# Performance work log

Hardware: AMD Instinct MI355X
Metric: run time of the kernel (lower is better)

## Reference

```python
import jax, jax.numpy as jnp
import numpy as np
from jax import lax

B, C, H, W = 16, 256, 64, 64
K = 3  # kernel_size


def setup_inputs() -> dict:
    key = jax.random.key(0)
    k1, k2, k3, k4 = jax.random.split(key, 4)
    x = jax.random.normal(k1, (B, C, H, W), dtype=jnp.float32)
    # nn.Parameter init is ones; perturb so softmax is non-trivial
    dir_weight_h = jnp.ones((1, C, 1, 1), jnp.float32) + 0.1 * jax.random.normal(k2, (1, C, 1, 1), jnp.float32)
    dir_weight_w = jnp.ones((1, C, 1, 1), jnp.float32) + 0.1 * jax.random.normal(k3, (1, C, 1, 1), jnp.float32)
    gate_w = 0.1 * jax.random.normal(k4, (), jnp.float32)  # 1x1 conv on 1 channel = scalar
    gate_b = jnp.float32(-1.0)  # init.constant_(gate.bias, -1.0)
    return {"x": x, "dir_weight_h": dir_weight_h, "dir_weight_w": dir_weight_w,
            "gate_w": gate_w, "gate_b": gate_b}


def reference(x, dir_weight_h, dir_weight_w, gate_w, gate_b):
    b, c, h, w = x.shape
    # directional softmax-weighted global pooling
    ww = jax.nn.softmax(dir_weight_w, axis=1)            # (1,C,1,1)
    global_h = jnp.mean(x * ww, axis=3, keepdims=True)   # (B,C,H,1)
    wh = jax.nn.softmax(dir_weight_h, axis=1)
    global_w = jnp.mean(x * wh, axis=2, keepdims=True)   # (B,C,1,W)
    global_dir = global_h + global_w                     # broadcast -> (B,C,H,W)

    # local covariance: unfold(x1)*unfold(x2) mean over k*k taps
    # == KxK box-sum of (x1*x2) with zero padding, divided by k*k
    half = c // 2
    prod = x[:, :half] * x[:, half:]                     # (B,C/2,H,W)
    cov = lax.reduce_window(prod, 0.0, lax.add,
                            window_dimensions=(1, 1, K, K),
                            window_strides=(1, 1, 1, 1),
                            padding=[(0, 0), (0, 0), (K // 2, K // 2), (K // 2, K // 2)]) / (K * K)

    consistency = jnp.mean(jnp.abs(cov), axis=1, keepdims=True)  # (B,1,H,W)
    local_anomaly = 1.0 - jnp.clip(consistency, 0.0, 1.0)

    fusion = jnp.mean(global_dir, axis=1, keepdims=True) * local_anomaly  # (B,1,H,W)
    attention = jax.nn.sigmoid(gate_w * fusion + gate_b)  # 1x1 conv with scalar weight/bias
    return x * attention
```

## Files before the change

kernel.cpp:

```cpp
#include <hip/hip_runtime.h>
#include <math.h>

#define NB 16
#define NC 256
#define NH 64
#define NW 64
#define HALF 128
#define PLANE (NH*NW)

#define WS_ATT 0

#define SCR_CONS 0
#define SCR_GHP  524288
#define SCR_GWP  (524288 + 8192)

__device__ __forceinline__ float sum4(float4 v) { return (v.x+v.y)+(v.z+v.w); }

__global__ __launch_bounds__(256) void k_reduce(const float* __restrict__ x,
                                                const float* __restrict__ dwh,
                                                const float* __restrict__ dww,
                                                float* __restrict__ scr) {
    __shared__ float  ew[256], eh[256];
    __shared__ float  wsum[8];
    __shared__ float4 consacc[4][8][16];
    __shared__ float  ghacc[4][8];
    __shared__ float  gwacc[4][64];

    const int t    = threadIdx.x;
    const int v    = t >> 6;
    const int lane = t & 63;
    const int pl   = lane & 3;
    const int w4   = lane >> 2;

    const int blk = blockIdx.x;
    const int hg  = blk & 7;
    const int cg  = (blk >> 3) & 7;
    const int b   = blk >> 6;
    const int r0  = hg << 3;

    {
        const float vw = dww[t], vh = dwh[t];
        const float evw = expf(vw), evh = expf(vh);
        ew[t] = evw; eh[t] = evh;
        float sw = evw, sh = evh;
        #pragma unroll
        for (int m = 1; m < 64; m <<= 1) { sw += __shfl_xor(sw, m); sh += __shfl_xor(sh, m); }
        if (lane == 0) { wsum[v] = sw; wsum[4+v] = sh; }
    }
    __syncthreads();
    const float invSw = 1.f/((wsum[0]+wsum[1])+(wsum[2]+wsum[3]));
    const float invSh = 1.f/((wsum[4]+wsum[5])+(wsum[6]+wsum[7]));

    const int   c1  = cg*16 + v*4 + pl;
    const float ww1 = ew[c1]*invSw, ww2 = ew[c1+HALF]*invSw;
    const float wh1 = eh[c1]*invSh, wh2 = eh[c1+HALF]*invSh;

    const float* p1 = x + ((size_t)(b*NC + c1))*PLANE + w4*4;
    const float* p2 = p1 + (size_t)HALF*PLANE;

    float4 w0 = {0,0,0,0}, w1 = {0,0,0,0}, w2 = {0,0,0,0};
    float4 colacc = {0,0,0,0};

    #pragma unroll
    for (int j = 0; j < 10; ++j) {
        const int r = r0 - 1 + j;
        float4 p = {0.f,0.f,0.f,0.f};
        const bool live = (j == 0) ? (r >= 0) : ((j == 9) ? (r < 64) : true);
        if (live) {
            const float4 x1 = *reinterpret_cast<const float4*>(p1 + r*NW);
            const float4 x2 = *reinterpret_cast<const float4*>(p2 + r*NW);
            p.x = x1.x*x2.x; p.y = x1.y*x2.y; p.z = x1.z*x2.z; p.w = x1.w*x2.w;
            if (j >= 1 && j <= 8) {
                float g = ww1*sum4(x1) + ww2*sum4(x2);
                g += __shfl_xor(g,1);  g += __shfl_xor(g,2);  g += __shfl_xor(g,4);
                g += __shfl_xor(g,8);  g += __shfl_xor(g,16); g += __shfl_xor(g,32);
                if (lane == 0) ghacc[v][j-1] = g;
                colacc.x += wh1*x1.x + wh2*x2.x;
                colacc.y += wh1*x1.y + wh2*x2.y;
                colacc.z += wh1*x1.z + wh2*x2.z;
                colacc.w += wh1*x1.w + wh2*x2.w;
            }
        }
        w0 = w1; w1 = w2; w2 = p;
        if (j >= 2) {
            float4 vs;
            vs.x = w0.x+w1.x+w2.x; vs.y = w0.y+w1.y+w2.y;
            vs.z = w0.z+w1.z+w2.z; vs.w = w0.w+w1.w+w2.w;
            float L = __shfl_up(vs.w, 4);
            float R = __shfl_down(vs.x, 4);
            if (w4 == 0)  L = 0.f;
            if (w4 == 15) R = 0.f;
            float4 c;
            c.x = fabsf(L    + vs.x + vs.y);
            c.y = fabsf(vs.x + vs.y + vs.z);
            c.z = fabsf(vs.y + vs.z + vs.w);
            c.w = fabsf(vs.z + vs.w + R);
            c.x += __shfl_xor(c.x,1); c.x += __shfl_xor(c.x,2);
            c.y += __shfl_xor(c.y,1); c.y += __shfl_xor(c.y,2);
            c.z += __shfl_xor(c.z,1); c.z += __shfl_xor(c.z,2);
            c.w += __shfl_xor(c.w,1); c.w += __shfl_xor(c.w,2);
            if (pl == 0) consacc[v][j-2][w4] = c;
        }
    }

    colacc.x += __shfl_xor(colacc.x,1); colacc.x += __shfl_xor(colacc.x,2);
    colacc.y += __shfl_xor(colacc.y,1); colacc.y += __shfl_xor(colacc.y,2);
    colacc.z += __shfl_xor(colacc.z,1); colacc.z += __shfl_xor(colacc.z,2);
    colacc.w += __shfl_xor(colacc.w,1); colacc.w += __shfl_xor(colacc.w,2);
    if (pl == 0) {
        gwacc[v][w4*4+0] = colacc.x;
        gwacc[v][w4*4+1] = colacc.y;
        gwacc[v][w4*4+2] = colacc.z;
        gwacc[v][w4*4+3] = colacc.w;
    }
    __syncthreads();

    const float SC  = 1.0f/(9.0f*128.0f);
    const float GSC = 1.0f/16384.0f;
    if (t < 128) {
        const int row = t >> 4, q = t & 15;
        const float4 s0 = consacc[0][row][q], s1 = consacc[1][row][q];
        const float4 s2 = consacc[2][row][q], s3 = consacc[3][row][q];
        float4 s;
        s.x = ((s0.x+s1.x)+(s2.x+s3.x))*SC;
        s.y = ((s0.y+s1.y)+(s2.y+s3.y))*SC;
        s.z = ((s0.z+s1.z)+(s2.z+s3.z))*SC;
        s.w = ((s0.w+s1.w)+(s2.w+s3.w))*SC;
        reinterpret_cast<float4*>(scr)[(cg << 14) + (b << 10) + (r0 + row)*16 + q] = s;
    } else if (t < 136) {
        const int row = t - 128;
        const float g = (ghacc[0][row]+ghacc[1][row])+(ghacc[2][row]+ghacc[3][row]);
        scr[SCR_GHP + (b*NH + r0 + row)*8 + cg] = g * GSC;
    } else if (t < 200) {
        const int w = t - 136;
        const float s = (gwacc[0][w]+gwacc[1][w])+(gwacc[2][w]+gwacc[3][w]);
        scr[SCR_GWP + (size_t)(b*NW + w)*64 + cg*8 + hg] = s * GSC;
    }
}

__global__ __launch_bounds__(256) void k_att(float* __restrict__ ws,
                                             const float* __restrict__ scr,
                                             const float* __restrict__ pgw,
                                             const float* __restrict__ pgb) {
    __shared__ __align__(16) float sgw[64];
    __shared__ __align__(16) float sgh[4];
    const int t = threadIdx.x;
    const int s = blockIdx.x & 15;
    const int b = blockIdx.x >> 4;

    if (t < 64) {
        const float4* gp = reinterpret_cast<const float4*>(scr + SCR_GWP + (size_t)(b*NW + t)*64);
        float acc = 0.f;
        #pragma unroll
        for (int i = 0; i < 16; ++i) acc += sum4(gp[i]);
        sgw[t] = acc;
    } else if (t < 68) {
        const int r = s*4 + (t - 64);
        const float4* gp = reinterpret_cast<const float4*>(scr + SCR_GHP + (b*NH + r)*8);
        sgh[t-64] = sum4(gp[0]) + sum4(gp[1]);
    }
    __syncthreads();

    if (t < 64) {
        const int u = (b << 10) + (s << 6) + t;
        const float4* cp = reinterpret_cast<const float4*>(scr);
        float4 sm = {0.f,0.f,0.f,0.f};
        #pragma unroll
        for (int g = 0; g < 8; ++g) {
            const float4 vv = cp[(g << 14) + u];
            sm.x += vv.x; sm.y += vv.y; sm.z += vv.z; sm.w += vv.w;
        }
        const float ghv  = sgh[t >> 4];
        const float4 gwv = *reinterpret_cast<const float4*>(&sgw[(t & 15)*4]);
        const float gW = pgw[0], gB = pgb[0];

        float4 o;
        float z;
        z = gW*(ghv+gwv.x)*(1.f - fminf(fmaxf(sm.x,0.f),1.f)) + gB; o.x = 1.f/(1.f+expf(-z));
        z = gW*(ghv+gwv.y)*(1.f - fminf(fmaxf(sm.y,0.f),1.f)) + gB; o.y = 1.f/(1.f+expf(-z));
        z = gW*(ghv+gwv.z)*(1.f - fminf(fmaxf(sm.z,0.f),1.f)) + gB; o.z = 1.f/(1.f+expf(-z));
        z = gW*(ghv+gwv.w)*(1.f - fminf(fmaxf(sm.w,0.f),1.f)) + gB; o.w = 1.f/(1.f+expf(-z));
        reinterpret_cast<float4*>(ws + WS_ATT)[u] = o;
    }
}

__global__ __launch_bounds__(256) void k_apply(const float* __restrict__ x,
                                               const float* __restrict__ ws,
                                               float* __restrict__ out) {
    const float* att = ws + WS_ATT;
    const int total4 = NB*NC*NH*NW/4;
    const int stride = gridDim.x * blockDim.x;
    for (int i = blockIdx.x*blockDim.x + threadIdx.x; i < total4; i += stride) {
        const int w4 = i & 15;
        const int h  = (i >> 4) & 63;
        const int b  = i >> 18;
        const float4 xv = reinterpret_cast<const float4*>(x)[i];
        const float4 av = reinterpret_cast<const float4*>(att)[(b << 10) + (h << 4) + w4];
        float4 o;
        o.x = xv.x*av.x; o.y = xv.y*av.y; o.z = xv.z*av.z; o.w = xv.w*av.w;
        reinterpret_cast<float4*>(out)[i] = o;
    }
}

extern "C" void kernel_launch(void* const* d_in, const int* in_sizes, int n_in,
                              void* d_out, int out_size, void* d_ws, size_t ws_size,
                              hipStream_t stream) {
    const float* x   = (const float*)d_in[0];
    const float* dwh = (const float*)d_in[1];
    const float* dww = (const float*)d_in[2];
    const float* pgw = (const float*)d_in[3];
    const float* pgb = (const float*)d_in[4];
    float* out = (float*)d_out;
    float* ws  = (float*)d_ws;
    float* scr = out;

    k_reduce<<<NB*8*8, 256, 0, stream>>>(x, dwh, dww, scr);
    k_att<<<256, 256, 0, stream>>>(ws, scr, pgw, pgb);
    k_apply<<<2048, 256, 0, stream>>>(x, ws, out);
}
```

Measured before the change: 43.68 us.

## Split channel pairs across lanes and double reduce grid to 2048 blocks

Each lane now loads one channel instead of both halves of a pair. The partner channel's value is obtained through a lane shuffle, and the per-block channel group shrinks from 16 to 8 channels. The reduce grid doubles to 2048 blocks to raise parallelism and memory-level concurrency on the first pass. In exchange, the scratch partial buffers and the attention kernel's reductions double in size (16 consistency groups, 128 column partials), which adds extra scratch traffic and shuffles.

```diff
diff --git a/kernel.cpp b/kernel.cpp
--- a/kernel.cpp
+++ b/kernel.cpp
@@ -11,8 +11,8 @@
 #define WS_ATT 0
 
 #define SCR_CONS 0
-#define SCR_GHP  524288
-#define SCR_GWP  (524288 + 8192)
+#define SCR_GHP  1048576
+#define SCR_GWP  (1048576 + 16384)
 
 __device__ __forceinline__ float sum4(float4 v) { return (v.x+v.y)+(v.z+v.w); }
 
@@ -29,13 +29,13 @@
     const int t    = threadIdx.x;
     const int v    = t >> 6;
     const int lane = t & 63;
-    const int pl   = lane & 3;
+    const int ch   = lane & 3;
     const int w4   = lane >> 2;
 
     const int blk = blockIdx.x;
     const int hg  = blk & 7;
-    const int cg  = (blk >> 3) & 7;
-    const int b   = blk >> 6;
+    const int cg  = (blk >> 3) & 15;
+    const int b   = blk >> 7;
     const int r0  = hg << 3;
 
     {
@@ -51,12 +51,11 @@
     const float invSw = 1.f/((wsum[0]+wsum[1])+(wsum[2]+wsum[3]));
     const float invSh = 1.f/((wsum[4]+wsum[5])+(wsum[6]+wsum[7]));
 
-    const int   c1  = cg*16 + v*4 + pl;
-    const float ww1 = ew[c1]*invSw, ww2 = ew[c1+HALF]*invSw;
-    const float wh1 = eh[c1]*invSh, wh2 = eh[c1+HALF]*invSh;
-
-    const float* p1 = x + ((size_t)(b*NC + c1))*PLANE + w4*4;
-    const float* p2 = p1 + (size_t)HALF*PLANE;
+    const int   c  = cg*8 + v*2 + (ch >> 1) + (ch & 1)*HALF;
+    const float wwc = ew[c]*invSw;
+    const float whc = eh[c]*invSh;
+
+    const float* pc = x + ((size_t)(b*NC + c))*PLANE + w4*4;
 
     float4 w0 = {0,0,0,0}, w1 = {0,0,0,0}, w2 = {0,0,0,0};
     float4 colacc = {0,0,0,0};
@@ -67,18 +66,20 @@
         float4 p = {0.f,0.f,0.f,0.f};
         const bool live = (j == 0) ? (r >= 0) : ((j == 9) ? (r < 64) : true);
         if (live) {
-            const float4 x1 = *reinterpret_cast<const float4*>(p1 + r*NW);
-            const float4 x2 = *reinterpret_cast<const float4*>(p2 + r*NW);
-            p.x = x1.x*x2.x; p.y = x1.y*x2.y; p.z = x1.z*x2.z; p.w = x1.w*x2.w;
+            const float4 xv = *reinterpret_cast<const float4*>(pc + r*NW);
+            float4 xp;
+            xp.x = __shfl_xor(xv.x, 1); xp.y = __shfl_xor(xv.y, 1);
+            xp.z = __shfl_xor(xv.z, 1); xp.w = __shfl_xor(xv.w, 1);
+            p.x = xv.x*xp.x; p.y = xv.y*xp.y; p.z = xv.z*xp.z; p.w = xv.w*xp.w;
             if (j >= 1 && j <= 8) {
-                float g = ww1*sum4(x1) + ww2*sum4(x2);
+                float g = wwc * sum4(xv);
                 g += __shfl_xor(g,1);  g += __shfl_xor(g,2);  g += __shfl_xor(g,4);
                 g += __shfl_xor(g,8);  g += __shfl_xor(g,16); g += __shfl_xor(g,32);
                 if (lane == 0) ghacc[v][j-1] = g;
-                colacc.x += wh1*x1.x + wh2*x2.x;
-                colacc.y += wh1*x1.y + wh2*x2.y;
-                colacc.z += wh1*x1.z + wh2*x2.z;
-                colacc.w += wh1*x1.w + wh2*x2.w;
+                colacc.x += whc*xv.x;
+                colacc.y += whc*xv.y;
+                colacc.z += whc*xv.z;
+                colacc.w += whc*xv.w;
             }
         }
         w0 = w1; w1 = w2; w2 = p;
@@ -90,16 +91,16 @@
             float R = __shfl_down(vs.x, 4);
             if (w4 == 0)  L = 0.f;
             if (w4 == 15) R = 0.f;
-            float4 c;
-            c.x = fabsf(L    + vs.x + vs.y);
-            c.y = fabsf(vs.x + vs.y + vs.z);
-            c.z = fabsf(vs.y + vs.z + vs.w);
-            c.w = fabsf(vs.z + vs.w + R);
-            c.x += __shfl_xor(c.x,1); c.x += __shfl_xor(c.x,2);
-            c.y += __shfl_xor(c.y,1); c.y += __shfl_xor(c.y,2);
-            c.z += __shfl_xor(c.z,1); c.z += __shfl_xor(c.z,2);
-            c.w += __shfl_xor(c.w,1); c.w += __shfl_xor(c.w,2);
-            if (pl == 0) consacc[v][j-2][w4] = c;
+            float4 cc;
+            cc.x = fabsf(L    + vs.x + vs.y);
+            cc.y = fabsf(vs.x + vs.y + vs.z);
+            cc.z = fabsf(vs.y + vs.z + vs.w);
+            cc.w = fabsf(vs.z + vs.w + R);
+            cc.x += __shfl_xor(cc.x,2);
+            cc.y += __shfl_xor(cc.y,2);
+            cc.z += __shfl_xor(cc.z,2);
+            cc.w += __shfl_xor(cc.w,2);
+            if (ch == 0) consacc[v][j-2][w4] = cc;
         }
     }
 
@@ -107,7 +108,7 @@
     colacc.y += __shfl_xor(colacc.y,1); colacc.y += __shfl_xor(colacc.y,2);
     colacc.z += __shfl_xor(colacc.z,1); colacc.z += __shfl_xor(colacc.z,2);
     colacc.w += __shfl_xor(colacc.w,1); colacc.w += __shfl_xor(colacc.w,2);
-    if (pl == 0) {
+    if (ch == 0) {
         gwacc[v][w4*4+0] = colacc.x;
         gwacc[v][w4*4+1] = colacc.y;
         gwacc[v][w4*4+2] = colacc.z;
@@ -130,11 +131,11 @@
     } else if (t < 136) {
         const int row = t - 128;
         const float g = (ghacc[0][row]+ghacc[1][row])+(ghacc[2][row]+ghacc[3][row]);
-        scr[SCR_GHP + (b*NH + r0 + row)*8 + cg] = g * GSC;
+        scr[SCR_GHP + (b*NH + r0 + row)*16 + cg] = g * GSC;
     } else if (t < 200) {
         const int w = t - 136;
         const float s = (gwacc[0][w]+gwacc[1][w])+(gwacc[2][w]+gwacc[3][w]);
-        scr[SCR_GWP + (size_t)(b*NW + w)*64 + cg*8 + hg] = s * GSC;
+        scr[SCR_GWP + (size_t)(b*NW + w)*128 + cg*8 + hg] = s * GSC;
     }
 }
 
@@ -149,15 +150,15 @@
     const int b = blockIdx.x >> 4;
 
     if (t < 64) {
-        const float4* gp = reinterpret_cast<const float4*>(scr + SCR_GWP + (size_t)(b*NW + t)*64);
+        const float4* gp = reinterpret_cast<const float4*>(scr + SCR_GWP + (size_t)(b*NW + t)*128);
         float acc = 0.f;
         #pragma unroll
-        for (int i = 0; i < 16; ++i) acc += sum4(gp[i]);
+        for (int i = 0; i < 32; ++i) acc += sum4(gp[i]);
         sgw[t] = acc;
     } else if (t < 68) {
         const int r = s*4 + (t - 64);
-        const float4* gp = reinterpret_cast<const float4*>(scr + SCR_GHP + (b*NH + r)*8);
-        sgh[t-64] = sum4(gp[0]) + sum4(gp[1]);
+        const float4* gp = reinterpret_cast<const float4*>(scr + SCR_GHP + (b*NH + r)*16);
+        sgh[t-64] = (sum4(gp[0]) + sum4(gp[1])) + (sum4(gp[2]) + sum4(gp[3]));
     }
     __syncthreads();
 
@@ -166,7 +167,7 @@
         const float4* cp = reinterpret_cast<const float4*>(scr);
         float4 sm = {0.f,0.f,0.f,0.f};
         #pragma unroll
-        for (int g = 0; g < 8; ++g) {
+        for (int g = 0; g < 16; ++g) {
             const float4 vv = cp[(g << 14) + u];
             sm.x += vv.x; sm.y += vv.y; sm.z += vv.z; sm.w += vv.w;
         }
@@ -214,7 +215,7 @@
     float* ws  = (float*)d_ws;
     float* scr = out;
 
-    k_reduce<<<NB*8*8, 256, 0, stream>>>(x, dwh, dww, scr);
+    k_reduce<<<NB*16*8, 256, 0, stream>>>(x, dwh, dww, scr);
     k_att<<<256, 256, 0, stream>>>(ws, scr, pgw, pgb);
     k_apply<<<2048, 256, 0, stream>>>(x, ws, out);
 }
```

Result: slower. 51.47 us (+17.8%).

## Restructure reduce kernel to process whole channel-pair planes per block via LDS stencil

Applied to the files above, without the earlier changes.

The reduce kernel now has each block process four full 64x64 channel-pair planes instead of an 8-row strip of 16 pairs. The horizontal 3-tap sum is done with lane shuffles, and the vertical sum goes through an LDS buffer. This removes halo row reloads and the per-row cross-lane reductions. The cost is four times more partial-sum planes in scratch, which the attention kernel now reduces over 32 groups, plus two barriers per plane.

```diff
diff --git a/kernel.cpp b/kernel.cpp
--- a/kernel.cpp
+++ b/kernel.cpp
@@ -7,36 +7,48 @@
 #define NW 64
 #define HALF 128
 #define PLANE (NH*NW)
+#define NPG 32
 
 #define WS_ATT 0
 
 #define SCR_CONS 0
-#define SCR_GHP  524288
-#define SCR_GWP  (524288 + 8192)
+#define SCR_GHP  2097152
+#define SCR_GWP  (2097152 + 32768)
+
+#define HPAD 76
 
 __device__ __forceinline__ float sum4(float4 v) { return (v.x+v.y)+(v.z+v.w); }
+
+__device__ __forceinline__ float4 hsum4(float4 p, int fc) {
+    float pl = __shfl_up(p.w, 1);
+    float pr = __shfl_down(p.x, 1);
+    if (fc == 0)  pl = 0.f;
+    if (fc == 15) pr = 0.f;
+    float4 h;
+    h.x = pl  + p.x + p.y;
+    h.y = p.x + p.y + p.z;
+    h.z = p.y + p.z + p.w;
+    h.w = p.z + p.w + pr;
+    return h;
+}
 
 __global__ __launch_bounds__(256) void k_reduce(const float* __restrict__ x,
                                                 const float* __restrict__ dwh,
                                                 const float* __restrict__ dww,
                                                 float* __restrict__ scr) {
-    __shared__ float  ew[256], eh[256];
-    __shared__ float  wsum[8];
-    __shared__ float4 consacc[4][8][16];
-    __shared__ float  ghacc[4][8];
-    __shared__ float  gwacc[4][64];
-
-    const int t    = threadIdx.x;
-    const int v    = t >> 6;
-    const int lane = t & 63;
-    const int pl   = lane & 3;
-    const int w4   = lane >> 2;
+    __shared__ float ew[256], eh[256];
+    __shared__ float wsum[8];
+    __shared__ float hs[64*HPAD];
+
+    const int t   = threadIdx.x;
+    const int v   = t >> 6;
+    const int lane= t & 63;
+    const int g16 = t >> 4;
+    const int w4  = t & 15;
 
     const int blk = blockIdx.x;
-    const int hg  = blk & 7;
-    const int cg  = (blk >> 3) & 7;
-    const int b   = blk >> 6;
-    const int r0  = hg << 3;
+    const int pg  = blk & (NPG-1);
+    const int b   = blk >> 5;
 
     {
         const float vw = dww[t], vh = dwh[t];
@@ -51,90 +63,118 @@
     const float invSw = 1.f/((wsum[0]+wsum[1])+(wsum[2]+wsum[3]));
     const float invSh = 1.f/((wsum[4]+wsum[5])+(wsum[6]+wsum[7]));
 
-    const int   c1  = cg*16 + v*4 + pl;
-    const float ww1 = ew[c1]*invSw, ww2 = ew[c1+HALF]*invSw;
-    const float wh1 = eh[c1]*invSh, wh2 = eh[c1+HALF]*invSh;
-
-    const float* p1 = x + ((size_t)(b*NC + c1))*PLANE + w4*4;
-    const float* p2 = p1 + (size_t)HALF*PLANE;
-
-    float4 w0 = {0,0,0,0}, w1 = {0,0,0,0}, w2 = {0,0,0,0};
+    float4 c4a0 = {0,0,0,0}, c4a1 = {0,0,0,0}, c4a2 = {0,0,0,0}, c4a3 = {0,0,0,0};
+    float  gh0 = 0.f, gh1 = 0.f, gh2 = 0.f, gh3 = 0.f;
     float4 colacc = {0,0,0,0};
+    float4* hsf4 = reinterpret_cast<float4*>(hs);
 
     #pragma unroll
-    for (int j = 0; j < 10; ++j) {
-        const int r = r0 - 1 + j;
-        float4 p = {0.f,0.f,0.f,0.f};
-        const bool live = (j == 0) ? (r >= 0) : ((j == 9) ? (r < 64) : true);
-        if (live) {
-            const float4 x1 = *reinterpret_cast<const float4*>(p1 + r*NW);
-            const float4 x2 = *reinterpret_cast<const float4*>(p2 + r*NW);
-            p.x = x1.x*x2.x; p.y = x1.y*x2.y; p.z = x1.z*x2.z; p.w = x1.w*x2.w;
-            if (j >= 1 && j <= 8) {
-                float g = ww1*sum4(x1) + ww2*sum4(x2);
-                g += __shfl_xor(g,1);  g += __shfl_xor(g,2);  g += __shfl_xor(g,4);
-                g += __shfl_xor(g,8);  g += __shfl_xor(g,16); g += __shfl_xor(g,32);
-                if (lane == 0) ghacc[v][j-1] = g;
-                colacc.x += wh1*x1.x + wh2*x2.x;
-                colacc.y += wh1*x1.y + wh2*x2.y;
-                colacc.z += wh1*x1.z + wh2*x2.z;
-                colacc.w += wh1*x1.w + wh2*x2.w;
-            }
-        }
-        w0 = w1; w1 = w2; w2 = p;
-        if (j >= 2) {
-            float4 vs;
-            vs.x = w0.x+w1.x+w2.x; vs.y = w0.y+w1.y+w2.y;
-            vs.z = w0.z+w1.z+w2.z; vs.w = w0.w+w1.w+w2.w;
-            float L = __shfl_up(vs.w, 4);
-            float R = __shfl_down(vs.x, 4);
-            if (w4 == 0)  L = 0.f;
-            if (w4 == 15) R = 0.f;
-            float4 c;
-            c.x = fabsf(L    + vs.x + vs.y);
-            c.y = fabsf(vs.x + vs.y + vs.z);
-            c.z = fabsf(vs.y + vs.z + vs.w);
-            c.w = fabsf(vs.z + vs.w + R);
-            c.x += __shfl_xor(c.x,1); c.x += __shfl_xor(c.x,2);
-            c.y += __shfl_xor(c.y,1); c.y += __shfl_xor(c.y,2);
-            c.z += __shfl_xor(c.z,1); c.z += __shfl_xor(c.z,2);
-            c.w += __shfl_xor(c.w,1); c.w += __shfl_xor(c.w,2);
-            if (pl == 0) consacc[v][j-2][w4] = c;
-        }
-    }
-
-    colacc.x += __shfl_xor(colacc.x,1); colacc.x += __shfl_xor(colacc.x,2);
-    colacc.y += __shfl_xor(colacc.y,1); colacc.y += __shfl_xor(colacc.y,2);
-    colacc.z += __shfl_xor(colacc.z,1); colacc.z += __shfl_xor(colacc.z,2);
-    colacc.w += __shfl_xor(colacc.w,1); colacc.w += __shfl_xor(colacc.w,2);
-    if (pl == 0) {
-        gwacc[v][w4*4+0] = colacc.x;
-        gwacc[v][w4*4+1] = colacc.y;
-        gwacc[v][w4*4+2] = colacc.z;
-        gwacc[v][w4*4+3] = colacc.w;
-    }
-    __syncthreads();
+    for (int pp = 0; pp < 4; ++pp) {
+        const int c1 = pg*4 + pp;
+        const float ww1 = ew[c1]*invSw, ww2 = ew[c1+HALF]*invSw;
+        const float wh1 = eh[c1]*invSh, wh2 = eh[c1+HALF]*invSh;
+
+        const float4* q1 = reinterpret_cast<const float4*>(x + ((size_t)(b*NC + c1))*PLANE);
+        const float4* q2 = reinterpret_cast<const float4*>(x + ((size_t)(b*NC + c1 + HALF))*PLANE);
+
+        const float4 a0 = q1[t], a1 = q1[t+256], a2 = q1[t+512], a3 = q1[t+768];
+        const float4 b0 = q2[t], b1 = q2[t+256], b2 = q2[t+512], b3 = q2[t+768];
+
+        gh0 += ww1*sum4(a0) + ww2*sum4(b0);
+        gh1 += ww1*sum4(a1) + ww2*sum4(b1);
+        gh2 += ww1*sum4(a2) + ww2*sum4(b2);
+        gh3 += ww1*sum4(a3) + ww2*sum4(b3);
+        colacc.x += wh1*((a0.x+a1.x)+(a2.x+a3.x)) + wh2*((b0.x+b1.x)+(b2.x+b3.x));
+        colacc.y += wh1*((a0.y+a1.y)+(a2.y+a3.y)) + wh2*((b0.y+b1.y)+(b2.y+b3.y));
+        colacc.z += wh1*((a0.z+a1.z)+(a2.z+a3.z)) + wh2*((b0.z+b1.z)+(b2.z+b3.z));
+        colacc.w += wh1*((a0.w+a1.w)+(a2.w+a3.w)) + wh2*((b0.w+b1.w)+(b2.w+b3.w));
+
+        float4 p, h;
+        p.x=a0.x*b0.x; p.y=a0.y*b0.y; p.z=a0.z*b0.z; p.w=a0.w*b0.w;
+        h = hsum4(p, w4); hsf4[(g16 +  0)*19 + w4] = h;
+        p.x=a1.x*b1.x; p.y=a1.y*b1.y; p.z=a1.z*b1.z; p.w=a1.w*b1.w;
+        h = hsum4(p, w4); hsf4[(g16 + 16)*19 + w4] = h;
+        p.x=a2.x*b2.x; p.y=a2.y*b2.y; p.z=a2.z*b2.z; p.w=a2.w*b2.w;
+        h = hsum4(p, w4); hsf4[(g16 + 32)*19 + w4] = h;
+        p.x=a3.x*b3.x; p.y=a3.y*b3.y; p.z=a3.z*b3.z; p.w=a3.w*b3.w;
+        h = hsum4(p, w4); hsf4[(g16 + 48)*19 + w4] = h;
+
+        __syncthreads();
+
+        {
+            const int r = g16;
+            const float4 mid = hsf4[r*19 + w4];
+            float4 top = {0,0,0,0}, bot;
+            if (r > 0) top = hsf4[(r-1)*19 + w4];
+            bot = hsf4[(r+1)*19 + w4];
+            c4a0.x += fabsf(top.x+mid.x+bot.x); c4a0.y += fabsf(top.y+mid.y+bot.y);
+            c4a0.z += fabsf(top.z+mid.z+bot.z); c4a0.w += fabsf(top.w+mid.w+bot.w);
+        }
+        {
+            const int r = g16 + 16;
+            const float4 mid = hsf4[r*19 + w4];
+            const float4 top = hsf4[(r-1)*19 + w4];
+            const float4 bot = hsf4[(r+1)*19 + w4];
+            c4a1.x += fabsf(top.x+mid.x+bot.x); c4a1.y += fabsf(top.y+mid.y+bot.y);
+            c4a1.z += fabsf(top.z+mid.z+bot.z); c4a1.w += fabsf(top.w+mid.w+bot.w);
+        }
+        {
+            const int r = g16 + 32;
+            const float4 mid = hsf4[r*19 + w4];
+            const float4 top = hsf4[(r-1)*19 + w4];
+            const float4 bot = hsf4[(r+1)*19 + w4];
+            c4a2.x += fabsf(top.x+mid.x+bot.x); c4a2.y += fabsf(top.y+mid.y+bot.y);
+            c4a2.z += fabsf(top.z+mid.z+bot.z); c4a2.w += fabsf(top.w+mid.w+bot.w);
+        }
+        {
+            const int r = g16 + 48;
+            const float4 mid = hsf4[r*19 + w4];
+            const float4 top = hsf4[(r-1)*19 + w4];
+            float4 bot = {0,0,0,0};
+            if (r < 63) bot = hsf4[(r+1)*19 + w4];
+            c4a3.x += fabsf(top.x+mid.x+bot.x); c4a3.y += fabsf(top.y+mid.y+bot.y);
+            c4a3.z += fabsf(top.z+mid.z+bot.z); c4a3.w += fabsf(top.w+mid.w+bot.w);
+        }
+
+        __syncthreads();
+    }
 
     const float SC  = 1.0f/(9.0f*128.0f);
     const float GSC = 1.0f/16384.0f;
-    if (t < 128) {
-        const int row = t >> 4, q = t & 15;
-        const float4 s0 = consacc[0][row][q], s1 = consacc[1][row][q];
-        const float4 s2 = consacc[2][row][q], s3 = consacc[3][row][q];
+
+    {
+        float4* dst = reinterpret_cast<float4*>(scr) + ((size_t)pg << 14) + (b << 10);
         float4 s;
-        s.x = ((s0.x+s1.x)+(s2.x+s3.x))*SC;
-        s.y = ((s0.y+s1.y)+(s2.y+s3.y))*SC;
-        s.z = ((s0.z+s1.z)+(s2.z+s3.z))*SC;
-        s.w = ((s0.w+s1.w)+(s2.w+s3.w))*SC;
-        reinterpret_cast<float4*>(scr)[(cg << 14) + (b << 10) + (r0 + row)*16 + q] = s;
-    } else if (t < 136) {
-        const int row = t - 128;
-        const float g = (ghacc[0][row]+ghacc[1][row])+(ghacc[2][row]+ghacc[3][row]);
-        scr[SCR_GHP + (b*NH + r0 + row)*8 + cg] = g * GSC;
-    } else if (t < 200) {
-        const int w = t - 136;
-        const float s = (gwacc[0][w]+gwacc[1][w])+(gwacc[2][w]+gwacc[3][w]);
-        scr[SCR_GWP + (size_t)(b*NW + w)*64 + cg*8 + hg] = s * GSC;
+        s.x=c4a0.x*SC; s.y=c4a0.y*SC; s.z=c4a0.z*SC; s.w=c4a0.w*SC; dst[(g16+ 0)*16 + w4] = s;
+        s.x=c4a1.x*SC; s.y=c4a1.y*SC; s.z=c4a1.z*SC; s.w=c4a1.w*SC; dst[(g16+16)*16 + w4] = s;
+        s.x=c4a2.x*SC; s.y=c4a2.y*SC; s.z=c4a2.z*SC; s.w=c4a2.w*SC; dst[(g16+32)*16 + w4] = s;
+        s.x=c4a3.x*SC; s.y=c4a3.y*SC; s.z=c4a3.z*SC; s.w=c4a3.w*SC; dst[(g16+48)*16 + w4] = s;
+    }
+
+    {
+        float* ghdst = scr + SCR_GHP + (size_t)(b*NPG + pg)*64;
+        float g;
+        g = gh0; g += __shfl_xor(g,1); g += __shfl_xor(g,2); g += __shfl_xor(g,4); g += __shfl_xor(g,8);
+        if (w4 == 0) ghdst[g16 +  0] = g * GSC;
+        g = gh1; g += __shfl_xor(g,1); g += __shfl_xor(g,2); g += __shfl_xor(g,4); g += __shfl_xor(g,8);
+        if (w4 == 0) ghdst[g16 + 16] = g * GSC;
+        g = gh2; g += __shfl_xor(g,1); g += __shfl_xor(g,2); g += __shfl_xor(g,4); g += __shfl_xor(g,8);
+        if (w4 == 0) ghdst[g16 + 32] = g * GSC;
+        g = gh3; g += __shfl_xor(g,1); g += __shfl_xor(g,2); g += __shfl_xor(g,4); g += __shfl_xor(g,8);
+        if (w4 == 0) ghdst[g16 + 48] = g * GSC;
+    }
+
+    hsf4[t] = colacc;
+    __syncthreads();
+    if (t < 16) {
+        float4 s = {0,0,0,0};
+        #pragma unroll
+        for (int g = 0; g < 16; ++g) {
+            const float4 vv = hsf4[g*16 + t];
+            s.x += vv.x; s.y += vv.y; s.z += vv.z; s.w += vv.w;
+        }
+        s.x *= GSC; s.y *= GSC; s.z *= GSC; s.w *= GSC;
+        *reinterpret_cast<float4*>(scr + SCR_GWP + (size_t)(b*NPG + pg)*64 + t*4) = s;
     }
 }
 
@@ -149,15 +189,18 @@
     const int b = blockIdx.x >> 4;
 
     if (t < 64) {
-        const float4* gp = reinterpret_cast<const float4*>(scr + SCR_GWP + (size_t)(b*NW + t)*64);
         float acc = 0.f;
-        #pragma unroll
-        for (int i = 0; i < 16; ++i) acc += sum4(gp[i]);
+        #pragma unroll 8
+        for (int pg = 0; pg < NPG; ++pg)
+            acc += scr[SCR_GWP + (size_t)(b*NPG + pg)*64 + t];
         sgw[t] = acc;
     } else if (t < 68) {
         const int r = s*4 + (t - 64);
-        const float4* gp = reinterpret_cast<const float4*>(scr + SCR_GHP + (b*NH + r)*8);
-        sgh[t-64] = sum4(gp[0]) + sum4(gp[1]);
+        float acc = 0.f;
+        #pragma unroll 8
+        for (int pg = 0; pg < NPG; ++pg)
+            acc += scr[SCR_GHP + (size_t)(b*NPG + pg)*64 + r];
+        sgh[t-64] = acc;
     }
     __syncthreads();
 
@@ -166,8 +209,8 @@
         const float4* cp = reinterpret_cast<const float4*>(scr);
         float4 sm = {0.f,0.f,0.f,0.f};
         #pragma unroll
-        for (int g = 0; g < 8; ++g) {
-            const float4 vv = cp[(g << 14) + u];
+        for (int g = 0; g < NPG; ++g) {
+            const float4 vv = cp[((size_t)g << 14) + u];
             sm.x += vv.x; sm.y += vv.y; sm.z += vv.z; sm.w += vv.w;
         }
         const float ghv  = sgh[t >> 4];
@@ -214,7 +257,7 @@
     float* ws  = (float*)d_ws;
     float* scr = out;
 
-    k_reduce<<<NB*8*8, 256, 0, stream>>>(x, dwh, dww, scr);
+    k_reduce<<<NB*NPG, 256, 0, stream>>>(x, dwh, dww, scr);
     k_att<<<256, 256, 0, stream>>>(ws, scr, pgw, pgb);
     k_apply<<<2048, 256, 0, stream>>>(x, ws, out);
 }
```

After: 50.43 us. 15.5% more time.
